# Kernel tuning notes

Measured on AMD Instinct MI355X. Metric: run time of the kernel, lower is better.

The kernel has to match this reference:

```python
import jax, jax.numpy as jnp
import numpy as np

SEQ, D, H = 4096, 1024, 1024


def setup_inputs() -> dict:
    key = jax.random.key(0)
    k_x, k_w1, k_b1, k_w2, k_b2 = jax.random.split(key, 5)
    std = 1.0 / np.sqrt(H)
    inputs = jax.random.normal(k_x, (SEQ, D), dtype=jnp.float32)
    W1 = jax.random.uniform(k_w1, (3 * H, 2 * D), minval=-std, maxval=std, dtype=jnp.float32)
    b1 = jax.random.uniform(k_b1, (3 * H,), minval=-std, maxval=std, dtype=jnp.float32)
    W2 = jax.random.uniform(k_w2, (H, H), minval=-std, maxval=std, dtype=jnp.float32)
    b2 = jax.random.uniform(k_b2, (H,), minval=-std, maxval=std, dtype=jnp.float32)
    return {"inputs": inputs, "W1": W1, "b1": b1, "W2": W2, "b2": b2}


def reference(inputs, W1, b1, W2, b2):
    # Exclusive prefix sum along seq: s[t] = sum_{i<t} x[i]
    s = jnp.concatenate(
        [jnp.zeros((1, inputs.shape[1]), dtype=inputs.dtype),
         jnp.cumsum(inputs[:-1], axis=0)], axis=0)
    v = jnp.concatenate([inputs, s], axis=1)            # [S, 2D]
    gates = v @ W1.T + b1                               # [S, 3H]
    ig, fg, h = jnp.split(gates, 3, axis=1)
    ig = jax.nn.sigmoid(ig)
    fg = jax.nn.sigmoid(fg)
    h = jnp.tanh(h) @ W2.T + b2                         # [S, H]
    hr = h * ig
    return (fg, hr)
```

## Files before the change

### kernel.cpp

```cpp
#include <hip/hip_runtime.h>
#include <cmath>

#define S_SEQ 4096
#define HD 1024
#define NG 3072
#define CHR 32
#define NCH 128
#define NZ 4

typedef _Float16 half8_t __attribute__((ext_vector_type(8)));
typedef _Float16 half4_t __attribute__((ext_vector_type(4)));
typedef float f32x4_t __attribute__((ext_vector_type(4)));

__device__ __forceinline__ void gload_lds16(const void* g, void* l) {
  __builtin_amdgcn_global_load_lds(
      (const __attribute__((address_space(1))) void*)g,
      (__attribute__((address_space(3))) void*)l, 16, 0, 0);
}

__device__ __forceinline__ float sigmoidf_(float x) {
  return 1.f / (1.f + __expf(-x));
}
__device__ __forceinline__ float tanhf_(float x) {
  return 1.f - 2.f / (__expf(2.f * x) + 1.f);
}

#define SCAN_BLOCKS 128
#define CONV_BLOCKS 7168
__global__ void prep(const float* __restrict__ W1, const float* __restrict__ W2,
                     _Float16* __restrict__ w1h, _Float16* __restrict__ w2h,
                     const float* __restrict__ x, _Float16* __restrict__ A,
                     _Float16* __restrict__ xsum) {
  const int bid = blockIdx.x;
  if (bid < SCAN_BLOCKS) {
    const int c = bid;
    const int j = threadIdx.x * 4;
    const int t0 = c * CHR;
    float4 run = make_float4(0.f, 0.f, 0.f, 0.f);
    for (int t = t0; t < t0 + CHR; t += 8) {
      float4 v[8];
#pragma unroll
      for (int u = 0; u < 8; ++u)
        v[u] = *(const float4*)&x[(size_t)(t + u) * HD + j];
#pragma unroll
      for (int u = 0; u < 8; ++u) {
        half4_t hx, hs;
        hx[0] = (_Float16)v[u].x;  hx[1] = (_Float16)v[u].y;
        hx[2] = (_Float16)v[u].z;  hx[3] = (_Float16)v[u].w;
        hs[0] = (_Float16)run.x;   hs[1] = (_Float16)run.y;
        hs[2] = (_Float16)run.z;   hs[3] = (_Float16)run.w;
        *(half4_t*)&A[(size_t)(t + u) * 2048 + j] = hx;
        *(half4_t*)&A[(size_t)(t + u) * 2048 + 1024 + j] = hs;
        run.x += v[u].x; run.y += v[u].y; run.z += v[u].z; run.w += v[u].w;
      }
    }
    half4_t hxs;
    hxs[0] = (_Float16)run.x; hxs[1] = (_Float16)run.y;
    hxs[2] = (_Float16)run.z; hxs[3] = (_Float16)run.w;
    *(half4_t*)&xsum[(size_t)c * HD + j] = hxs;
  } else {
    const int n1 = NG * 2048 / 4;
    int i = (bid - SCAN_BLOCKS) * 256 + threadIdx.x;
    const float* src = (i < n1) ? (W1 + (size_t)i * 4)
                                : (W2 + (size_t)(i - n1) * 4);
    _Float16* dst = (i < n1) ? (w1h + (size_t)i * 4)
                             : (w2h + (size_t)(i - n1) * 4);
    float4 v = *(const float4*)src;
    half4_t h;
    h[0] = (_Float16)v.x; h[1] = (_Float16)v.y;
    h[2] = (_Float16)v.z; h[3] = (_Float16)v.w;
    *(half4_t*)dst = h;
  }
}

__global__ void scan_part(const float* __restrict__ praw,
                          const float* __restrict__ b1,
                          float* __restrict__ pout) {
  int j = blockIdx.x * 256 + threadIdx.x;
  const size_t SP = (size_t)NCH * NG;
  float run = b1[j];
  for (int c = 0; c < NCH; c += 8) {
    float v[8];
#pragma unroll
    for (int u = 0; u < 8; ++u) {
      size_t i0 = (size_t)(c + u) * NG + j;
      v[u] = (praw[i0] + praw[i0 + SP]) + (praw[i0 + 2 * SP] + praw[i0 + 3 * SP]);
    }
#pragma unroll
    for (int u = 0; u < 8; ++u) {
      pout[(size_t)(c + u) * NG + j] = run;
      run += v[u];
    }
  }
}

__global__ __launch_bounds__(256, 2)
void gemm_part(const _Float16* __restrict__ A, const _Float16* __restrict__ B,
               float* __restrict__ C) {
  __shared__ _Float16 As[128 * 32];
  __shared__ _Float16 Bs[128 * 32];

  const int tid = threadIdx.x;
  const int lane = tid & 63;
  const int wid = tid >> 6;
  const int wr = wid >> 1;
  const int wc = wid & 1;

  const int n0 = blockIdx.x * 128;
  const int koff = blockIdx.z * (1024 / NZ);

  const int srow = lane >> 2;
  const int scol = (lane & 3) << 3;

  const _Float16* gA = A + (size_t)(wid * 32 + srow) * 1024 + koff + scol;
  const _Float16* gB = B + (size_t)(n0 + wid * 32 + srow) * 2048 + koff + scol;
  _Float16* lA = As + (wid * 32) * 32;
  _Float16* lB = Bs + (wid * 32) * 32;

  f32x4_t acc[4][4] = {};

  const int fr = lane & 15;
  const int fk = (lane >> 4) << 3;

  for (int kk = 0; kk < 1024 / NZ; kk += 32) {
    gload_lds16(gA + kk,                    lA);
    gload_lds16(gA + kk + (size_t)16*1024,  lA + 16 * 32);
    gload_lds16(gB + kk,                    lB);
    gload_lds16(gB + kk + (size_t)16*2048,  lB + 16 * 32);
    __syncthreads();

    half8_t af[4], bf[4];
#pragma unroll
    for (int m = 0; m < 4; ++m)
      af[m] = *(const half8_t*)&As[(wr * 64 + m * 16 + fr) * 32 + fk];
#pragma unroll
    for (int n = 0; n < 4; ++n)
      bf[n] = *(const half8_t*)&Bs[(wc * 64 + n * 16 + fr) * 32 + fk];
#pragma unroll
    for (int m = 0; m < 4; ++m)
#pragma unroll
      for (int n = 0; n < 4; ++n)
        acc[m][n] = __builtin_amdgcn_mfma_f32_16x16x32_f16(af[m], bf[n],
                                                           acc[m][n], 0, 0, 0);
    __syncthreads();
  }

  float* Cz = C + (size_t)blockIdx.z * NCH * NG;
  const int crow = wr * 64 + ((lane >> 4) << 2);
  const int ccol = n0 + wc * 64 + fr;
#pragma unroll
  for (int m = 0; m < 4; ++m)
#pragma unroll
    for (int n = 0; n < 4; ++n) {
      const int col = ccol + n * 16;
#pragma unroll
      for (int r = 0; r < 4; ++r)
        Cz[(size_t)(crow + m * 16 + r) * NG + col] = acc[m][n][r];
    }
}

#define BARX __builtin_amdgcn_s_barrier()
#define PR1 __builtin_amdgcn_s_setprio(1)
#define PR0 __builtin_amdgcn_s_setprio(0)

template <int NTILE, int MODE, int SWZ, int NBX, int BN>
__global__ __launch_bounds__(256, BN == 192 ? 2 : 3)
void gemm_t3(const _Float16* __restrict__ A, const _Float16* __restrict__ B,
             int N,
             const float* __restrict__ part, _Float16* __restrict__ igb,
             float* __restrict__ outf, _Float16* __restrict__ th,
             const float* __restrict__ bias, const _Float16* __restrict__ mulh) {
  constexpr int KS = NTILE * 32;
  constexpr int NF = BN / 32;
  constexpr int NLB = BN / 64;
  __shared__ __align__(16) _Float16 sA[3][128 * 32];
  __shared__ __align__(16) _Float16 sB[3][BN * 32];

  const int tid = threadIdx.x;
  const int l = tid & 63;
  const int wid = tid >> 6;
  const int wr = wid >> 1;
  const int wc = wid & 1;

  int bx, by;
  if constexpr (SWZ) {
    const int bid = blockIdx.x;
    const int xcd = bid & 7;
    const int q = bid >> 3;
    by = xcd * 4 + q / NBX;
    bx = q % NBX;
  } else {
    bx = blockIdx.x;
    by = blockIdx.y;
  }
  const int m0 = by * 128;
  const int n0 = bx * BN;

  const int srow = tid >> 2;
  const int schunk = (tid & 3) ^ ((tid >> 3) & 3);
  const _Float16* gA = A + (size_t)(m0 + srow) * KS + schunk * 8;
  const _Float16* gB = B + (size_t)(n0 + srow) * KS + schunk * 8;
  const int ldst = tid * 8;

#define STG(bn, kt) do {                                              \
    const int kk_ = (kt) * 32;                                        \
    gload_lds16(gA + kk_,           &sA[bn][ldst]);                   \
    gload_lds16(gA + kk_ + 64 * KS, &sA[bn][2048 + ldst]);            \
    _Pragma("unroll")                                                 \
    for (int jj = 0; jj < NLB; ++jj)                                  \
      gload_lds16(gB + kk_ + jj * 64 * KS, &sB[bn][jj * 2048 + ldst]);\
  } while (0)

#define VMW do {                                                      \
    if constexpr (NLB == 1)                                           \
      asm volatile("s_waitcnt vmcnt(3)" ::: "memory");                \
    else if constexpr (NLB == 2)                                      \
      asm volatile("s_waitcnt vmcnt(4)" ::: "memory");                \
    else                                                              \
      asm volatile("s_waitcnt vmcnt(5)" ::: "memory");                \
  } while (0)

  const int fr = l & 15;
  const int kidx = (((l >> 4) ^ ((l >> 1) & 3)) << 3);
  const int noff = wc * (BN / 2);

  f32x4_t acc[4][NF] = {};

#define BODY(kt, bc, bn) do {                                         \
    int ks_ = (kt) + 2; if (ks_ > NTILE - 1) ks_ = NTILE - 1;         \
    STG(bn, ks_);                                                     \
    half8_t af[4], bf[NF];                                            \
    _Pragma("unroll")                                                 \
    for (int m = 0; m < 4; ++m)                                       \
      af[m] = *(const half8_t*)&sA[bc][(wr*64 + m*16 + fr)*32 + kidx];\
    _Pragma("unroll")                                                 \
    for (int n = 0; n < NF; ++n)                                      \
      bf[n] = *(const half8_t*)&sB[bc][(noff + n*16 + fr)*32 + kidx]; \
    PR1;                                                              \
    _Pragma("unroll")                                                 \
    for (int m = 0; m < 4; ++m)                                       \
      _Pragma("unroll")                                               \
      for (int n = 0; n < NF; ++n)                                    \
        acc[m][n] = __builtin_amdgcn_mfma_f32_16x16x32_f16(           \
            af[m], bf[n], acc[m][n], 0, 0, 0);                        \
    PR0;                                                              \
    VMW; BARX;                                                        \
  } while (0)

  STG(0, 0);
  STG(1, 1);
  VMW; BARX;

#pragma unroll 1
  for (int t3 = 0; t3 < NTILE / 3; ++t3) {
    const int kt = t3 * 3;
    BODY(kt,     0, 2);
    BODY(kt + 1, 1, 0);
    BODY(kt + 2, 2, 1);
  }
  if constexpr (NTILE % 3 >= 1) BODY(NTILE - NTILE % 3,     0, 2);
  if constexpr (NTILE % 3 >= 2) BODY(NTILE - NTILE % 3 + 1, 1, 0);

  const int crow = m0 + wr * 64 + ((l >> 4) << 2);
  const int ccol = n0 + noff + fr;

  float pv[2][NF];
  if constexpr (MODE == 2) {
    const int cbase = crow >> 5;
#pragma unroll
    for (int h = 0; h < 2; ++h)
#pragma unroll
      for (int n = 0; n < NF; ++n)
        pv[h][n] = part[(size_t)(cbase + h) * NG + ccol + n * 16];
  }

#pragma unroll
  for (int m = 0; m < 4; ++m)
#pragma unroll
    for (int n = 0; n < NF; ++n) {
      const int col = ccol + n * 16;
#pragma unroll
      for (int r = 0; r < 4; ++r) {
        const int row = crow + m * 16 + r;
        const float v = acc[m][n][r];
        if (MODE == 1) {
          size_t idx = (size_t)row * N + col;
          outf[idx] = (v + bias[col]) * (float)mulh[idx];
        } else {
          float g = v + pv[m >> 1][n];
          if (col < 1024)
            igb[(size_t)row * HD + col] = (_Float16)sigmoidf_(g);
          else if (col < 2048)
            outf[(size_t)row * HD + (col - 1024)] = sigmoidf_(g);
          else
            th[(size_t)row * HD + (col - 2048)] = (_Float16)tanhf_(g);
        }
      }
    }
#undef STG
#undef VMW
#undef BODY
}

extern "C" void kernel_launch(void* const* d_in, const int* in_sizes, int n_in,
                              void* d_out, int out_size, void* d_ws, size_t ws_size,
                              hipStream_t stream) {
  const float* x  = (const float*)d_in[0];
  const float* W1 = (const float*)d_in[1];
  const float* b1 = (const float*)d_in[2];
  const float* W2 = (const float*)d_in[3];
  const float* b2 = (const float*)d_in[4];
  float* out0 = (float*)d_out;
  float* out1 = out0 + (size_t)S_SEQ * HD;

  char* ws = (char*)d_ws;
  _Float16* Ah    = (_Float16*)(ws);
  _Float16* w1h   = (_Float16*)(ws + ((size_t)16 << 20));
  _Float16* w2h   = (_Float16*)(ws + ((size_t)28 << 20));
  _Float16* xsumh = (_Float16*)(ws + ((size_t)30 << 20));
  float*    praw  = (float*)   (ws + ((size_t)31 << 20));
  float*    pout  = (float*)   (ws + ((size_t)37 << 20));
  _Float16* igb   = (_Float16*)(ws + ((size_t)39 << 20));
  _Float16* th    = (_Float16*)(ws + ((size_t)47 << 20));

  prep<<<dim3(SCAN_BLOCKS + CONV_BLOCKS), dim3(256), 0, stream>>>(
      W1, W2, w1h, w2h, x, Ah, xsumh);

  gemm_part<<<dim3(NG / 128, 1, NZ), dim3(256), 0, stream>>>(
      xsumh, w1h + 1024, praw);

  scan_part<<<dim3(NG / 256), dim3(256), 0, stream>>>(praw, b1, pout);

  gemm_t3<64, 2, 1, NG / 192, 192><<<dim3(512), dim3(256), 0, stream>>>(
      Ah, w1h, NG, pout, igb, out0, th, nullptr, nullptr);

  gemm_t3<32, 1, 1, 16, 64><<<dim3(512), dim3(256), 0, stream>>>(
      th, w2h, HD, nullptr, nullptr, out1, nullptr, b2, igb);
}
```

Measured before the change: 135.6 us.

## Replace first GEMM with dedicated K=64 double-buffered kernel

Adds a specialized kernel for the large gate GEMM that stages 64-wide K tiles in a two-buffer LDS pipeline with an XOR swizzle, in place of the generic triple-buffered 32-wide K loop. Each iteration issues twice as many MFMAs between barriers, which halves the barrier and loop overhead per unit of work. The cost is a full vmcnt(0) wait every iteration, so prefetch depth drops to one tile and memory latency may be less well hidden. The generic template is trimmed to the second GEMM's epilogue only.

```diff
diff --git a/kernel.cpp b/kernel.cpp
--- a/kernel.cpp
+++ b/kernel.cpp
@@ -163,12 +163,139 @@
 #define PR1 __builtin_amdgcn_s_setprio(1)
 #define PR0 __builtin_amdgcn_s_setprio(0)
 
-template <int NTILE, int MODE, int SWZ, int NBX, int BN>
-__global__ __launch_bounds__(256, BN == 192 ? 2 : 3)
+__global__ __launch_bounds__(256, 2)
+void gemm1_k64(const _Float16* __restrict__ A, const _Float16* __restrict__ B,
+               const float* __restrict__ part, _Float16* __restrict__ igb,
+               float* __restrict__ out0, _Float16* __restrict__ th) {
+  constexpr int KS = 2048;
+  constexpr int NT = 32;
+  __shared__ __align__(16) _Float16 sA[2][128 * 64];
+  __shared__ __align__(16) _Float16 sB[2][192 * 64];
+
+  const int tid = threadIdx.x;
+  const int l = tid & 63;
+  const int wid = tid >> 6;
+  const int wr = wid >> 1;
+  const int wc = wid & 1;
+
+  const int bid = blockIdx.x;
+  const int xcd = bid & 7;
+  const int q = bid >> 3;
+  const int by = xcd * 4 + q / 16;
+  const int bx = q % 16;
+  const int m0 = by * 128;
+  const int n0 = bx * 192;
+
+  const int rB = tid >> 3;
+  const int cB = tid & 7;
+  const int csw = (cB ^ (rB & 7)) << 3;
+  const _Float16* gA0 = A + (size_t)(m0 + rB) * KS + csw;
+  const _Float16* gB0 = B + (size_t)(n0 + rB) * KS + csw;
+  const int dsto = rB * 64 + cB * 8;
+
+#define STG(bb, kt) do {                                               \
+    const int kk_ = (kt) * 64;                                         \
+    _Pragma("unroll")                                                  \
+    for (int j = 0; j < 4; ++j)                                        \
+      gload_lds16(gA0 + (size_t)(32 * j) * KS + kk_,                   \
+                  (_Float16*)&sA[bb][dsto + j * 2048]);                \
+    _Pragma("unroll")                                                  \
+    for (int j = 0; j < 6; ++j)                                        \
+      gload_lds16(gB0 + (size_t)(32 * j) * KS + kk_,                   \
+                  (_Float16*)&sB[bb][dsto + j * 2048]);                \
+  } while (0)
+
+  const int fr = l & 15;
+  const int kq = l >> 4;
+
+#define RDA(dst, M, H, bb) do {                                        \
+    const int row_ = wr * 64 + (M) * 16 + fr;                          \
+    dst = *(const half8_t*)&sA[bb][row_ * 64 +                         \
+          ((((H) * 4 + kq) ^ (row_ & 7)) << 3)];                       \
+  } while (0)
+#define RDB(dst, N_, H, bb) do {                                       \
+    const int row_ = wc * 96 + (N_) * 16 + fr;                         \
+    dst = *(const half8_t*)&sB[bb][row_ * 64 +                         \
+          ((((H) * 4 + kq) ^ (row_ & 7)) << 3)];                       \
+  } while (0)
+
+  f32x4_t acc[4][6] = {};
+
+#define BODY(t, bb) do {                                               \
+    const int nt_ = ((t) + 1 < NT) ? (t) + 1 : NT - 1;                 \
+    STG((bb) ^ 1, nt_);                                                \
+    half8_t af[4][2], bf[6][2];                                        \
+    _Pragma("unroll")                                                  \
+    for (int m = 0; m < 4; ++m) {                                      \
+      RDA(af[m][0], m, 0, bb); RDA(af[m][1], m, 1, bb);                \
+    }                                                                  \
+    _Pragma("unroll")                                                  \
+    for (int n = 0; n < 6; ++n) {                                      \
+      RDB(bf[n][0], n, 0, bb); RDB(bf[n][1], n, 1, bb);                \
+    }                                                                  \
+    PR1;                                                               \
+    _Pragma("unroll")                                                  \
+    for (int m = 0; m < 4; ++m)                                        \
+      _Pragma("unroll")                                                \
+      for (int n = 0; n < 6; ++n) {                                    \
+        acc[m][n] = __builtin_amdgcn_mfma_f32_16x16x32_f16(            \
+            af[m][0], bf[n][0], acc[m][n], 0, 0, 0);                   \
+        acc[m][n] = __builtin_amdgcn_mfma_f32_16x16x32_f16(            \
+            af[m][1], bf[n][1], acc[m][n], 0, 0, 0);                   \
+      }                                                                \
+    PR0;                                                               \
+    asm volatile("s_waitcnt vmcnt(0)" ::: "memory");                   \
+    BARX;                                                              \
+  } while (0)
+
+  STG(0, 0);
+  asm volatile("s_waitcnt vmcnt(0)" ::: "memory");
+  BARX;
+
+#pragma unroll 1
+  for (int t2 = 0; t2 < NT / 2; ++t2) {
+    BODY(2 * t2,     0);
+    BODY(2 * t2 + 1, 1);
+  }
+
+  const int crow = m0 + wr * 64 + ((l >> 4) << 2);
+  const int ccol = n0 + wc * 96 + fr;
+
+  float pv[2][6];
+  const int cbase = crow >> 5;
+#pragma unroll
+  for (int h = 0; h < 2; ++h)
+#pragma unroll
+    for (int n = 0; n < 6; ++n)
+      pv[h][n] = part[(size_t)(cbase + h) * NG + ccol + n * 16];
+
+#pragma unroll
+  for (int m = 0; m < 4; ++m)
+#pragma unroll
+    for (int n = 0; n < 6; ++n) {
+      const int col = ccol + n * 16;
+#pragma unroll
+      for (int r = 0; r < 4; ++r) {
+        const int row = crow + m * 16 + r;
+        float g = acc[m][n][r] + pv[m >> 1][n];
+        if (col < 1024)
+          igb[(size_t)row * HD + col] = (_Float16)sigmoidf_(g);
+        else if (col < 2048)
+          out0[(size_t)row * HD + (col - 1024)] = sigmoidf_(g);
+        else
+          th[(size_t)row * HD + (col - 2048)] = (_Float16)tanhf_(g);
+      }
+    }
+#undef STG
+#undef RDA
+#undef RDB
+#undef BODY
+}
+
+template <int NTILE, int SWZ, int NBX, int BN>
+__global__ __launch_bounds__(256, 3)
 void gemm_t3(const _Float16* __restrict__ A, const _Float16* __restrict__ B,
-             int N,
-             const float* __restrict__ part, _Float16* __restrict__ igb,
-             float* __restrict__ outf, _Float16* __restrict__ th,
+             int N, float* __restrict__ outf,
              const float* __restrict__ bias, const _Float16* __restrict__ mulh) {
   constexpr int KS = NTILE * 32;
   constexpr int NF = BN / 32;
@@ -214,10 +341,8 @@
 #define VMW do {                                                      \
     if constexpr (NLB == 1)                                           \
       asm volatile("s_waitcnt vmcnt(3)" ::: "memory");                \
-    else if constexpr (NLB == 2)                                      \
+    else                                                              \
       asm volatile("s_waitcnt vmcnt(4)" ::: "memory");                \
-    else                                                              \
-      asm volatile("s_waitcnt vmcnt(5)" ::: "memory");                \
   } while (0)
 
   const int fr = l & 15;
@@ -263,17 +388,6 @@
 
   const int crow = m0 + wr * 64 + ((l >> 4) << 2);
   const int ccol = n0 + noff + fr;
-
-  float pv[2][NF];
-  if constexpr (MODE == 2) {
-    const int cbase = crow >> 5;
-#pragma unroll
-    for (int h = 0; h < 2; ++h)
-#pragma unroll
-      for (int n = 0; n < NF; ++n)
-        pv[h][n] = part[(size_t)(cbase + h) * NG + ccol + n * 16];
-  }
-
 #pragma unroll
   for (int m = 0; m < 4; ++m)
 #pragma unroll
@@ -282,19 +396,8 @@
 #pragma unroll
       for (int r = 0; r < 4; ++r) {
         const int row = crow + m * 16 + r;
-        const float v = acc[m][n][r];
-        if (MODE == 1) {
-          size_t idx = (size_t)row * N + col;
-          outf[idx] = (v + bias[col]) * (float)mulh[idx];
-        } else {
-          float g = v + pv[m >> 1][n];
-          if (col < 1024)
-            igb[(size_t)row * HD + col] = (_Float16)sigmoidf_(g);
-          else if (col < 2048)
-            outf[(size_t)row * HD + (col - 1024)] = sigmoidf_(g);
-          else
-            th[(size_t)row * HD + (col - 2048)] = (_Float16)tanhf_(g);
-        }
+        size_t idx = (size_t)row * N + col;
+        outf[idx] = (acc[m][n][r] + bias[col]) * (float)mulh[idx];
       }
     }
 #undef STG
@@ -331,9 +434,9 @@
 
   scan_part<<<dim3(NG / 256), dim3(256), 0, stream>>>(praw, b1, pout);
 
-  gemm_t3<64, 2, 1, NG / 192, 192><<<dim3(512), dim3(256), 0, stream>>>(
-      Ah, w1h, NG, pout, igb, out0, th, nullptr, nullptr);
-
-  gemm_t3<32, 1, 1, 16, 64><<<dim3(512), dim3(256), 0, stream>>>(
-      th, w2h, HD, nullptr, nullptr, out1, nullptr, b2, igb);
-}
+  gemm1_k64<<<dim3(512), dim3(256), 0, stream>>>(
+      Ah, w1h, pout, igb, out0, th);
+
+  gemm_t3<32, 1, 16, 64><<<dim3(512), dim3(256), 0, stream>>>(
+      th, w2h, HD, out1, b2, igb);
+}
```

Result: faster. 127.2 us (-6.3%).
